# Performance work log

Hardware: AMD Instinct MI355X
Metric: run time of the kernel (lower is better)

Reference implementation:

```python
import jax, jax.numpy as jnp
import numpy as np

E, H, I, T, K = 32, 1024, 768, 2048, 8


def setup_inputs() -> dict:
    key = jax.random.key(0)
    ks = jax.random.split(key, 6)
    hidden_states = jax.random.normal(ks[0], (T, H), dtype=jnp.float32)
    routing_weights = jax.random.uniform(ks[1], (T, K), dtype=jnp.float32)
    selected_experts = jax.random.randint(ks[2], (T, K), 0, E, dtype=jnp.int32)
    scale = 0.02
    gate_proj = jax.random.normal(ks[3], (E, I, H), dtype=jnp.float32) * scale
    up_proj = jax.random.normal(ks[4], (E, I, H), dtype=jnp.float32) * scale
    down_proj = jax.random.normal(ks[5], (E, H, I), dtype=jnp.float32) * scale
    return {
        "hidden_states": hidden_states,
        "routing_weights": routing_weights,
        "selected_experts": selected_experts,
        "gate_proj": gate_proj,
        "up_proj": up_proj,
        "down_proj": down_proj,
    }


def reference(hidden_states, routing_weights, selected_experts, gate_proj, up_proj, down_proj):
    # hidden_states: [T, H]; routing_weights/selected_experts: [T, K]
    # gate/up: [E, I, H]; down: [E, H, I]
    T_, _ = hidden_states.shape
    E_ = gate_proj.shape[0]
    # combine[t, e] = sum_k routing_weights[t, k] * 1[selected_experts[t, k] == e]
    combine = jnp.zeros((T_, E_), hidden_states.dtype).at[
        jnp.arange(T_)[:, None], selected_experts
    ].add(routing_weights)
    g = jnp.einsum('th,eih->eti', hidden_states, gate_proj)   # [E, T, I]
    u = jnp.einsum('th,eih->eti', hidden_states, up_proj)     # [E, T, I]
    h = jax.nn.silu(g) * u                                    # SwiGLU
    d = jnp.einsum('eti,ehi->eth', h, down_proj)              # [E, T, H]
    out = jnp.einsum('eth,te->th', d, combine)                # weighted combine
    return out
```

## Files before the change

kernel.cpp:

```cpp
#include <hip/hip_runtime.h>
#include <hip/hip_bf16.h>
#include <math.h>

#define E_N 32
#define H_N 1024
#define I_N 768
#define T_N 2048
#define K_N 8
#define MT  128
#define NPAIRS (T_N * K_N)
#define MAX_SLOTS (NPAIRS + E_N * MT)
#define MAX_TILES (NPAIRS / MT + E_N)

typedef __attribute__((ext_vector_type(8))) short bf16x8;
typedef __attribute__((ext_vector_type(4))) short bf16x4;
typedef __attribute__((ext_vector_type(8))) float f32x8;
typedef __attribute__((ext_vector_type(4))) float f32x4;

__device__ __forceinline__ unsigned pk2(float a, float b) {
    unsigned ua = __float_as_uint(a) + 0x8000u;
    unsigned ub = __float_as_uint(b) + 0x8000u;
    return (ua >> 16) | (ub & 0xffff0000u);
}
__device__ __forceinline__ bf16x8 cvt8(f32x8 v) {
    union { unsigned u[4]; bf16x8 h; } r;
    r.u[0] = pk2(v[0], v[1]); r.u[1] = pk2(v[2], v[3]);
    r.u[2] = pk2(v[4], v[5]); r.u[3] = pk2(v[6], v[7]);
    return r.h;
}
__device__ __forceinline__ float bf2f(short s) {
    return __uint_as_float(((unsigned)(unsigned short)s) << 16);
}

__global__ void route_kernel(const int* __restrict__ sel,
                             int* __restrict__ slot_token,
                             int* __restrict__ pair_slot,
                             int* __restrict__ tile_expert,
                             int* __restrict__ tile_row0,
                             int* __restrict__ n_tiles_out) {
    __shared__ int cnt[E_N], off[E_N], cur[E_N];
    int tid = threadIdx.x;
    if (tid < E_N) cnt[tid] = 0;
    __syncthreads();
    for (int p = tid; p < NPAIRS; p += blockDim.x)
        atomicAdd(&cnt[sel[p]], 1);
    __syncthreads();
    if (tid == 0) {
        int acc = 0, tt = 0;
        for (int e = 0; e < E_N; ++e) {
            off[e] = acc;
            cur[e] = 0;
            int nt = (cnt[e] + MT - 1) / MT;
            for (int i = 0; i < nt; ++i) {
                tile_expert[tt] = e;
                tile_row0[tt] = acc + i * MT;
                ++tt;
            }
            acc += nt * MT;
        }
        *n_tiles_out = tt;
    }
    __syncthreads();
    for (int p = tid; p < NPAIRS; p += blockDim.x) {
        int e = sel[p];
        int slot = off[e] + atomicAdd(&cur[e], 1);
        slot_token[slot] = p / K_N;
        pair_slot[p] = slot;
    }
}

__global__ __launch_bounds__(256) void gather_kernel(
    const float* __restrict__ hs,
    const int* __restrict__ slot_token,
    short* __restrict__ x_buf) {
    int idx = blockIdx.x * 256 + threadIdx.x;
    int slot = idx >> 8;
    int pos = (idx & 255) * 4;
    int tok = slot_token[slot];
    union { unsigned u[2]; bf16x4 s; } o;
    if (tok >= 0) {
        f32x4 v = *(const f32x4*)(hs + (size_t)tok * H_N + pos);
        o.u[0] = pk2(v[0], v[1]);
        o.u[1] = pk2(v[2], v[3]);
    } else {
        o.u[0] = 0; o.u[1] = 0;
    }
    *(bf16x4*)(x_buf + (size_t)slot * H_N + pos) = o.s;
}

__global__ __launch_bounds__(256, 2) void gateup_kernel(
    const short* __restrict__ x_buf,
    const float* __restrict__ gate,
    const float* __restrict__ up,
    const int* __restrict__ tile_expert,
    const int* __restrict__ tile_row0,
    const int* __restrict__ n_tiles,
    __hip_bfloat16* __restrict__ h_buf) {
    int tile = blockIdx.x;
    if (tile >= *n_tiles) return;
    __shared__ short sA[128 * 32];
    __shared__ short sG[128 * 32];
    __shared__ short sU[128 * 32];
    int e = tile_expert[tile];
    int row0 = tile_row0[tile];
    int col0 = blockIdx.y * 128;
    int tid = threadIdx.x;
    int wave = tid >> 6, lane = tid & 63, quad = lane >> 4, r16 = lane & 15;
    int m0w = (wave >> 1) * 64, n0w = (wave & 1) * 64;
    int srow = tid >> 2;
    int scol = (tid & 3) * 8;

    f32x4 accG[4][4], accU[4][4];
#pragma unroll
    for (int i = 0; i < 4; ++i)
#pragma unroll
        for (int j = 0; j < 4; ++j) {
            accG[i][j] = (f32x4){0.f, 0.f, 0.f, 0.f};
            accU[i][j] = (f32x4){0.f, 0.f, 0.f, 0.f};
        }

    const size_t gbase = ((size_t)e * I_N + col0) * H_N;

#pragma unroll 1
    for (int k0 = 0; k0 < H_N; k0 += 32) {
        __syncthreads();
#pragma unroll
        for (int r = 0; r < 2; ++r) {
            int row = r * 64 + srow;
            bf16x8 av = *(const bf16x8*)(x_buf + (size_t)(row0 + row) * H_N + k0 + scol);
            *(bf16x8*)&sA[row * 32 + scol] = av;
            f32x8 gv = *(const f32x8*)(gate + gbase + (size_t)row * H_N + k0 + scol);
            *(bf16x8*)&sG[row * 32 + scol] = cvt8(gv);
            f32x8 uv = *(const f32x8*)(up + gbase + (size_t)row * H_N + k0 + scol);
            *(bf16x8*)&sU[row * 32 + scol] = cvt8(uv);
        }
        __syncthreads();
        bf16x8 af[4], bg[4], bu[4];
#pragma unroll
        for (int mi = 0; mi < 4; ++mi)
            af[mi] = *(const bf16x8*)&sA[(m0w + mi * 16 + r16) * 32 + quad * 8];
#pragma unroll
        for (int ni = 0; ni < 4; ++ni) {
            bg[ni] = *(const bf16x8*)&sG[(n0w + ni * 16 + r16) * 32 + quad * 8];
            bu[ni] = *(const bf16x8*)&sU[(n0w + ni * 16 + r16) * 32 + quad * 8];
        }
#pragma unroll
        for (int mi = 0; mi < 4; ++mi)
#pragma unroll
            for (int ni = 0; ni < 4; ++ni) {
                accG[mi][ni] = __builtin_amdgcn_mfma_f32_16x16x32_bf16(af[mi], bg[ni], accG[mi][ni], 0, 0, 0);
                accU[mi][ni] = __builtin_amdgcn_mfma_f32_16x16x32_bf16(af[mi], bu[ni], accU[mi][ni], 0, 0, 0);
            }
    }
#pragma unroll
    for (int mi = 0; mi < 4; ++mi)
#pragma unroll
        for (int ni = 0; ni < 4; ++ni)
#pragma unroll
            for (int r = 0; r < 4; ++r) {
                int m = m0w + mi * 16 + quad * 4 + r;
                int n = col0 + n0w + ni * 16 + r16;
                float g = accG[mi][ni][r], u = accU[mi][ni][r];
                float hval = g * u / (1.0f + __expf(-g));
                h_buf[(size_t)(row0 + m) * I_N + n] = __float2bfloat16(hval);
            }
}

__global__ __launch_bounds__(256, 2) void down_kernel(
    const __hip_bfloat16* __restrict__ h_buf,
    const float* __restrict__ down,
    const int* __restrict__ tile_expert,
    const int* __restrict__ tile_row0,
    const int* __restrict__ n_tiles,
    short* __restrict__ d_buf) {
    int tile = blockIdx.x;
    if (tile >= *n_tiles) return;
    __shared__ short sA[128 * 32];
    __shared__ short sB[128 * 32];
    int e = tile_expert[tile];
    int row0 = tile_row0[tile];
    int col0 = blockIdx.y * 128;
    int tid = threadIdx.x;
    int wave = tid >> 6, lane = tid & 63, quad = lane >> 4, r16 = lane & 15;
    int m0w = (wave >> 1) * 64, n0w = (wave & 1) * 64;
    int srow = tid >> 2;
    int scol = (tid & 3) * 8;

    f32x4 acc[4][4];
#pragma unroll
    for (int i = 0; i < 4; ++i)
#pragma unroll
        for (int j = 0; j < 4; ++j) acc[i][j] = (f32x4){0.f, 0.f, 0.f, 0.f};

    const short* hb = (const short*)h_buf;
    const size_t dbase = ((size_t)e * H_N + col0) * I_N;

#pragma unroll 1
    for (int k0 = 0; k0 < I_N; k0 += 32) {
        __syncthreads();
#pragma unroll
        for (int r = 0; r < 2; ++r) {
            int row = r * 64 + srow;
            bf16x8 av = *(const bf16x8*)(hb + (size_t)(row0 + row) * I_N + k0 + scol);
            *(bf16x8*)&sA[row * 32 + scol] = av;
            f32x8 bv = *(const f32x8*)(down + dbase + (size_t)row * I_N + k0 + scol);
            *(bf16x8*)&sB[row * 32 + scol] = cvt8(bv);
        }
        __syncthreads();
        bf16x8 af[4], bf[4];
#pragma unroll
        for (int mi = 0; mi < 4; ++mi)
            af[mi] = *(const bf16x8*)&sA[(m0w + mi * 16 + r16) * 32 + quad * 8];
#pragma unroll
        for (int ni = 0; ni < 4; ++ni)
            bf[ni] = *(const bf16x8*)&sB[(n0w + ni * 16 + r16) * 32 + quad * 8];
#pragma unroll
        for (int mi = 0; mi < 4; ++mi)
#pragma unroll
            for (int ni = 0; ni < 4; ++ni)
                acc[mi][ni] = __builtin_amdgcn_mfma_f32_16x16x32_bf16(af[mi], bf[ni], acc[mi][ni], 0, 0, 0);
    }
#pragma unroll
    for (int mi = 0; mi < 4; ++mi)
#pragma unroll
        for (int ni = 0; ni < 4; ++ni)
#pragma unroll
            for (int r = 0; r < 4; ++r) {
                int m = m0w + mi * 16 + quad * 4 + r;
                int n = col0 + n0w + ni * 16 + r16;
                unsigned u = __float_as_uint(acc[mi][ni][r]) + 0x8000u;
                d_buf[(size_t)(row0 + m) * H_N + n] = (short)(u >> 16);
            }
}

__global__ __launch_bounds__(256) void combine_kernel(
    const short* __restrict__ d_buf,
    const int* __restrict__ pair_slot,
    const float* __restrict__ rw,
    float* __restrict__ out) {
    int idx = blockIdx.x * blockDim.x + threadIdx.x;
    int t = idx >> 10;
    int h = idx & (H_N - 1);
    float acc = 0.f;
#pragma unroll
    for (int k = 0; k < K_N; ++k) {
        int slot = pair_slot[t * K_N + k];
        float w = rw[t * K_N + k];
        acc += w * bf2f(d_buf[(size_t)slot * H_N + h]);
    }
    out[idx] = acc;
}

extern "C" void kernel_launch(void* const* d_in, const int* in_sizes, int n_in,
                              void* d_out, int out_size, void* d_ws, size_t ws_size,
                              hipStream_t stream) {
    const float* hs   = (const float*)d_in[0];
    const float* rw   = (const float*)d_in[1];
    const int*   sel  = (const int*)d_in[2];
    const float* gate = (const float*)d_in[3];
    const float* up   = (const float*)d_in[4];
    const float* down = (const float*)d_in[5];
    float* out = (float*)d_out;

    char* ws = (char*)d_ws;
    int* slot_token  = (int*)ws;  ws += ((size_t)MAX_SLOTS * 4 + 255) / 256 * 256;
    int* pair_slot   = (int*)ws;  ws += ((size_t)NPAIRS * 4 + 255) / 256 * 256;
    int* tile_expert = (int*)ws;  ws += ((size_t)MAX_TILES * 4 + 255) / 256 * 256;
    int* tile_row0   = (int*)ws;  ws += ((size_t)MAX_TILES * 4 + 255) / 256 * 256;
    int* n_tiles     = (int*)ws;  ws += 256;
    short* x_buf = (short*)ws;    ws += ((size_t)MAX_SLOTS * H_N * 2 + 255) / 256 * 256;
    __hip_bfloat16* h_buf = (__hip_bfloat16*)ws;
    short* d_buf = x_buf;

    hipMemsetAsync(slot_token, 0xFF, (size_t)MAX_SLOTS * 4, stream);
    route_kernel<<<1, 256, 0, stream>>>(sel, slot_token, pair_slot,
                                        tile_expert, tile_row0, n_tiles);
    gather_kernel<<<(MAX_SLOTS * H_N / 4) / 256, 256, 0, stream>>>(hs, slot_token, x_buf);

    dim3 grid_gu(MAX_TILES, I_N / 128);
    gateup_kernel<<<grid_gu, 256, 0, stream>>>(x_buf, gate, up, tile_expert,
                                               tile_row0, n_tiles, h_buf);

    dim3 grid_dn(MAX_TILES, H_N / 128);
    down_kernel<<<grid_dn, 256, 0, stream>>>(h_buf, down, tile_expert,
                                             tile_row0, n_tiles, d_buf);

    combine_kernel<<<(T_N * H_N) / 256, 256, 0, stream>>>(d_buf, pair_slot,
                                                          rw, out);
}
```

Before: 521.7 us.

## Prefetch next K-slice into registers, pad LDS rows, remap blocks for XCD locality

Both grouped GEMM kernels now load the next K-slice of activations and weights into registers while the current slice is consumed by MFMAs, overlapping global loads with compute. LDS row stride is padded from 32 to 40 shorts to reduce bank conflicts on fragment reads. The 2D grid is flattened and remapped so that consecutive blocks on each of the 8 XCDs walk contiguous tiles, aiming to improve L2 reuse of weights. The register prefetch raises VGPR pressure, which may hurt occupancy under the launch bound of 2.

Result: faster. 495.6 us (-5.0%).

```diff
diff --git a/kernel.cpp b/kernel.cpp
--- a/kernel.cpp
+++ b/kernel.cpp
@@ -11,6 +11,7 @@
 #define NPAIRS (T_N * K_N)
 #define MAX_SLOTS (NPAIRS + E_N * MT)
 #define MAX_TILES (NPAIRS / MT + E_N)
+#define RS 40
 
 typedef __attribute__((ext_vector_type(8))) short bf16x8;
 typedef __attribute__((ext_vector_type(4))) short bf16x4;
@@ -96,14 +97,17 @@
     const int* __restrict__ tile_row0,
     const int* __restrict__ n_tiles,
     __hip_bfloat16* __restrict__ h_buf) {
-    int tile = blockIdx.x;
+    int id = blockIdx.x;
+    int W = (id & 7) * 120 + (id >> 3);
+    int tile = W % MAX_TILES;
+    int ycol = W / MAX_TILES;
     if (tile >= *n_tiles) return;
-    __shared__ short sA[128 * 32];
-    __shared__ short sG[128 * 32];
-    __shared__ short sU[128 * 32];
+    __shared__ short sA[128 * RS];
+    __shared__ short sG[128 * RS];
+    __shared__ short sU[128 * RS];
     int e = tile_expert[tile];
     int row0 = tile_row0[tile];
-    int col0 = blockIdx.y * 128;
+    int col0 = ycol * 128;
     int tid = threadIdx.x;
     int wave = tid >> 6, lane = tid & 63, quad = lane >> 4, r16 = lane & 15;
     int m0w = (wave >> 1) * 64, n0w = (wave & 1) * 64;
@@ -121,28 +125,45 @@
 
     const size_t gbase = ((size_t)e * I_N + col0) * H_N;
 
+    bf16x8 pa[2];
+    f32x8 pg[2], pu[2];
+#pragma unroll
+    for (int r = 0; r < 2; ++r) {
+        int row = r * 64 + srow;
+        pa[r] = *(const bf16x8*)(x_buf + (size_t)(row0 + row) * H_N + scol);
+        pg[r] = *(const f32x8*)(gate + gbase + (size_t)row * H_N + scol);
+        pu[r] = *(const f32x8*)(up + gbase + (size_t)row * H_N + scol);
+    }
+
 #pragma unroll 1
     for (int k0 = 0; k0 < H_N; k0 += 32) {
         __syncthreads();
 #pragma unroll
         for (int r = 0; r < 2; ++r) {
             int row = r * 64 + srow;
-            bf16x8 av = *(const bf16x8*)(x_buf + (size_t)(row0 + row) * H_N + k0 + scol);
-            *(bf16x8*)&sA[row * 32 + scol] = av;
-            f32x8 gv = *(const f32x8*)(gate + gbase + (size_t)row * H_N + k0 + scol);
-            *(bf16x8*)&sG[row * 32 + scol] = cvt8(gv);
-            f32x8 uv = *(const f32x8*)(up + gbase + (size_t)row * H_N + k0 + scol);
-            *(bf16x8*)&sU[row * 32 + scol] = cvt8(uv);
+            *(bf16x8*)&sA[row * RS + scol] = pa[r];
+            *(bf16x8*)&sG[row * RS + scol] = cvt8(pg[r]);
+            *(bf16x8*)&sU[row * RS + scol] = cvt8(pu[r]);
         }
         __syncthreads();
+        if (k0 + 32 < H_N) {
+            int kn = k0 + 32;
+#pragma unroll
+            for (int r = 0; r < 2; ++r) {
+                int row = r * 64 + srow;
+                pa[r] = *(const bf16x8*)(x_buf + (size_t)(row0 + row) * H_N + kn + scol);
+                pg[r] = *(const f32x8*)(gate + gbase + (size_t)row * H_N + kn + scol);
+                pu[r] = *(const f32x8*)(up + gbase + (size_t)row * H_N + kn + scol);
+            }
+        }
         bf16x8 af[4], bg[4], bu[4];
 #pragma unroll
         for (int mi = 0; mi < 4; ++mi)
-            af[mi] = *(const bf16x8*)&sA[(m0w + mi * 16 + r16) * 32 + quad * 8];
+            af[mi] = *(const bf16x8*)&sA[(m0w + mi * 16 + r16) * RS + quad * 8];
 #pragma unroll
         for (int ni = 0; ni < 4; ++ni) {
-            bg[ni] = *(const bf16x8*)&sG[(n0w + ni * 16 + r16) * 32 + quad * 8];
-            bu[ni] = *(const bf16x8*)&sU[(n0w + ni * 16 + r16) * 32 + quad * 8];
+            bg[ni] = *(const bf16x8*)&sG[(n0w + ni * 16 + r16) * RS + quad * 8];
+            bu[ni] = *(const bf16x8*)&sU[(n0w + ni * 16 + r16) * RS + quad * 8];
         }
 #pragma unroll
         for (int mi = 0; mi < 4; ++mi)
@@ -173,13 +194,16 @@
     const int* __restrict__ tile_row0,
     const int* __restrict__ n_tiles,
     short* __restrict__ d_buf) {
-    int tile = blockIdx.x;
+    int id = blockIdx.x;
+    int W = (id & 7) * 160 + (id >> 3);
+    int tile = W % MAX_TILES;
+    int ycol = W / MAX_TILES;
     if (tile >= *n_tiles) return;
-    __shared__ short sA[128 * 32];
-    __shared__ short sB[128 * 32];
+    __shared__ short sA[128 * RS];
+    __shared__ short sB[128 * RS];
     int e = tile_expert[tile];
     int row0 = tile_row0[tile];
-    int col0 = blockIdx.y * 128;
+    int col0 = ycol * 128;
     int tid = threadIdx.x;
     int wave = tid >> 6, lane = tid & 63, quad = lane >> 4, r16 = lane & 15;
     int m0w = (wave >> 1) * 64, n0w = (wave & 1) * 64;
@@ -195,25 +219,41 @@
     const short* hb = (const short*)h_buf;
     const size_t dbase = ((size_t)e * H_N + col0) * I_N;
 
+    bf16x8 pa[2];
+    f32x8 pb[2];
+#pragma unroll
+    for (int r = 0; r < 2; ++r) {
+        int row = r * 64 + srow;
+        pa[r] = *(const bf16x8*)(hb + (size_t)(row0 + row) * I_N + scol);
+        pb[r] = *(const f32x8*)(down + dbase + (size_t)row * I_N + scol);
+    }
+
 #pragma unroll 1
     for (int k0 = 0; k0 < I_N; k0 += 32) {
         __syncthreads();
 #pragma unroll
         for (int r = 0; r < 2; ++r) {
             int row = r * 64 + srow;
-            bf16x8 av = *(const bf16x8*)(hb + (size_t)(row0 + row) * I_N + k0 + scol);
-            *(bf16x8*)&sA[row * 32 + scol] = av;
-            f32x8 bv = *(const f32x8*)(down + dbase + (size_t)row * I_N + k0 + scol);
-            *(bf16x8*)&sB[row * 32 + scol] = cvt8(bv);
+            *(bf16x8*)&sA[row * RS + scol] = pa[r];
+            *(bf16x8*)&sB[row * RS + scol] = cvt8(pb[r]);
         }
         __syncthreads();
+        if (k0 + 32 < I_N) {
+            int kn = k0 + 32;
+#pragma unroll
+            for (int r = 0; r < 2; ++r) {
+                int row = r * 64 + srow;
+                pa[r] = *(const bf16x8*)(hb + (size_t)(row0 + row) * I_N + kn + scol);
+                pb[r] = *(const f32x8*)(down + dbase + (size_t)row * I_N + kn + scol);
+            }
+        }
         bf16x8 af[4], bf[4];
 #pragma unroll
         for (int mi = 0; mi < 4; ++mi)
-            af[mi] = *(const bf16x8*)&sA[(m0w + mi * 16 + r16) * 32 + quad * 8];
+            af[mi] = *(const bf16x8*)&sA[(m0w + mi * 16 + r16) * RS + quad * 8];
 #pragma unroll
         for (int ni = 0; ni < 4; ++ni)
-            bf[ni] = *(const bf16x8*)&sB[(n0w + ni * 16 + r16) * 32 + quad * 8];
+            bf[ni] = *(const bf16x8*)&sB[(n0w + ni * 16 + r16) * RS + quad * 8];
 #pragma unroll
         for (int mi = 0; mi < 4; ++mi)
 #pragma unroll
@@ -277,13 +317,11 @@
                                         tile_expert, tile_row0, n_tiles);
     gather_kernel<<<(MAX_SLOTS * H_N / 4) / 256, 256, 0, stream>>>(hs, slot_token, x_buf);
 
-    dim3 grid_gu(MAX_TILES, I_N / 128);
-    gateup_kernel<<<grid_gu, 256, 0, stream>>>(x_buf, gate, up, tile_expert,
-                                               tile_row0, n_tiles, h_buf);
-
-    dim3 grid_dn(MAX_TILES, H_N / 128);
-    down_kernel<<<grid_dn, 256, 0, stream>>>(h_buf, down, tile_expert,
-                                             tile_row0, n_tiles, d_buf);
+    gateup_kernel<<<MAX_TILES * (I_N / 128), 256, 0, stream>>>(
+        x_buf, gate, up, tile_expert, tile_row0, n_tiles, h_buf);
+
+    down_kernel<<<MAX_TILES * (H_N / 128), 256, 0, stream>>>(
+        h_buf, down, tile_expert, tile_row0, n_tiles, d_buf);
 
     combine_kernel<<<(T_N * H_N) / 256, 256, 0, stream>>>(d_buf, pair_slot,
                                                           rw, out);
```
